# Kernel tuning notes

Hardware: AMD Instinct MI355X
Metric: run time of the kernel (lower is better)

Reference implementation:

```python
import jax, jax.numpy as jnp
import numpy as np

B, S, D, H = 2, 2048, 1024, 16
HD = D // H  # 64


def setup_inputs() -> dict:
    key = jax.random.key(0)
    ks = jax.random.split(key, 11)
    sc = 1.0 / np.sqrt(D)
    return {
        "query": jax.random.normal(ks[0], (B, S, D), jnp.float32),
        "key_in": jax.random.normal(ks[1], (B, S, D), jnp.float32),
        "value_in": jax.random.normal(ks[2], (B, S, D), jnp.float32),
        "mask": jnp.ones((1, 1, S, S), dtype=bool),
        "Wq": jax.random.normal(ks[3], (D, D), jnp.float32) * sc,
        "bq": jnp.zeros((D,), jnp.float32),
        "Wk": jax.random.normal(ks[4], (D, D), jnp.float32) * sc,
        "bk": jnp.zeros((D,), jnp.float32),
        "Wv": jax.random.normal(ks[5], (D, D), jnp.float32) * sc,
        "bv": jnp.zeros((D,), jnp.float32),
        "Wo": jax.random.normal(ks[6], (D, D), jnp.float32) * sc,
        "bo": jnp.zeros((D,), jnp.float32),
    }


def _split_heads(x):
    b, s, _ = x.shape
    return x.reshape(b, s, H, HD).transpose(0, 2, 1, 3)  # [B,H,S,HD]


def reference(query, key_in, value_in, mask, Wq, bq, Wk, bk, Wv, bv, Wo, bo):
    # linear projections (torch Linear: x @ W.T + b)
    q = _split_heads(query @ Wq.T + bq)
    k = _split_heads(key_in @ Wk.T + bk)
    v = _split_heads(value_in @ Wv.T + bv)
    scores = jnp.einsum("bhqd,bhkd->bhqk", q, k) / np.sqrt(HD).astype(np.float32)
    scores = jnp.where(mask == 0, jnp.float32(-1e20), scores)
    probs = jax.nn.softmax(scores, axis=-1)
    attn = jnp.einsum("bhqk,bhkd->bhqd", probs, v)  # [B,H,S,HD]
    combined = attn.transpose(0, 2, 1, 3).reshape(query.shape[0], query.shape[1], H * HD)
    return combined @ Wo.T + bo
```

## Files before the change

### kernel.cpp

```cpp
#include <hip/hip_runtime.h>

#define B_  2
#define S_  2048
#define D_  1024
#define H_  16
#define HD_ 64

typedef float          f32x4 __attribute__((ext_vector_type(4)));
typedef short          s16x8 __attribute__((ext_vector_type(8)));
typedef unsigned short u16x4 __attribute__((ext_vector_type(4)));
typedef unsigned int   u32x4 __attribute__((ext_vector_type(4)));

static __device__ __forceinline__ unsigned short f2bf(float f) {
  unsigned int u = __builtin_bit_cast(unsigned int, f);
  u += 0x7FFFu + ((u >> 16) & 1u);
  return (unsigned short)(u >> 16);
}

#define GLDS16(g, l)                                                        \
  __builtin_amdgcn_global_load_lds(                                         \
      (const __attribute__((address_space(1))) void*)(g),                   \
      (__attribute__((address_space(3))) void*)(l), 16, 0, 0)

struct ConvSet {
  const float* s[4];
  unsigned short* d[4];
  int n[4];
};

__global__ __launch_bounds__(256) void conv_kernel(ConvSet cs) {
  const int idx = blockIdx.y;
  const int i = (blockIdx.x * 256 + threadIdx.x) * 8;
  if (i >= cs.n[idx]) return;
  const float* s = cs.s[idx];
  unsigned short* d = cs.d[idx];
  f32x4 a = *(const f32x4*)(s + i);
  f32x4 b = *(const f32x4*)(s + i + 4);
  u16x4 pa, pb;
#pragma unroll
  for (int j = 0; j < 4; ++j) { pa[j] = f2bf(a[j]); pb[j] = f2bf(b[j]); }
  *(u16x4*)(d + i) = pa;
  *(u16x4*)(d + i + 4) = pb;
}

template <int XM, bool PERM>
__global__ __launch_bounds__(256) void gemm_bf16(
    const void* __restrict__ X0, const void* __restrict__ X1,
    const void* __restrict__ X2,
    const unsigned short* __restrict__ W0, const unsigned short* __restrict__ W1,
    const unsigned short* __restrict__ W2,
    const float* __restrict__ b0, const float* __restrict__ b1, const float* __restrict__ b2,
    void* __restrict__ o0, void* __restrict__ o1, void* __restrict__ o2)
{
  constexpr int K = D_, N = D_;
  const int z = blockIdx.z;
  const void* X           = z == 0 ? X0 : (z == 1 ? X1 : X2);
  const unsigned short* W = z == 0 ? W0 : (z == 1 ? W1 : W2);
  const float* bias       = z == 0 ? b0 : (z == 1 ? b1 : b2);
  void* outp              = z == 0 ? o0 : (z == 1 ? o1 : o2);

  __shared__ unsigned short As[128][32];
  __shared__ unsigned short Bs[128][32];

  const int t = threadIdx.x, lane = t & 63, w = t >> 6;
  const int wr = w >> 1, wc = w & 1;
  const int Lb = blockIdx.y * 8 + blockIdx.x;
  const int m0 = (Lb & 31) * 128;
  const int n0 = (Lb >> 5) * 128;
  const int lg = lane >> 4, lr = lane & 15;

  const int srow = w * 32 + (lane >> 2);
  const int scol = (lane & 3) * 8;
  const unsigned short* Bsrc = W + (size_t)(n0 + srow) * K + scol;
  const unsigned short* Asrc =
      (XM == 0) ? (const unsigned short*)X + (size_t)(m0 + srow) * K + scol : nullptr;

  f32x4 acc[4][4];
#pragma unroll
  for (int i = 0; i < 4; ++i)
#pragma unroll
    for (int j = 0; j < 4; ++j) acc[i][j] = f32x4{0.f, 0.f, 0.f, 0.f};

  for (int k0 = 0; k0 < K; k0 += 32) {
    __syncthreads();
    if (XM == 0) {
#pragma unroll
      for (int i = 0; i < 2; ++i)
        GLDS16(Asrc + k0 + (size_t)i * 16 * K, &As[w * 32 + i * 16][0]);
    } else {
      const float* Xf = (const float*)X;
#pragma unroll
      for (int i = 0; i < 4; ++i) {
        int c = t + 256 * i;
        int row = c >> 3, ko = (c & 7) * 4;
        f32x4 v = *(const f32x4*)(Xf + (size_t)(m0 + row) * K + k0 + ko);
        u16x4 p;
#pragma unroll
        for (int j = 0; j < 4; ++j) p[j] = f2bf(v[j]);
        *(u16x4*)&As[row][ko] = p;
      }
    }
#pragma unroll
    for (int i = 0; i < 2; ++i)
      GLDS16(Bsrc + k0 + (size_t)i * 16 * K, &Bs[w * 32 + i * 16][0]);
    __syncthreads();

    s16x8 af[4], bfr[4];
#pragma unroll
    for (int i = 0; i < 4; ++i) af[i]  = *(const s16x8*)&As[wr * 64 + i * 16 + lr][lg * 8];
#pragma unroll
    for (int j = 0; j < 4; ++j) bfr[j] = *(const s16x8*)&Bs[wc * 64 + j * 16 + lr][lg * 8];
#pragma unroll
    for (int i = 0; i < 4; ++i)
#pragma unroll
      for (int j = 0; j < 4; ++j)
        acc[i][j] = __builtin_amdgcn_mfma_f32_16x16x32_bf16(af[i], bfr[j], acc[i][j], 0, 0, 0);
  }

#pragma unroll
  for (int i = 0; i < 4; ++i) {
    int rowb = m0 + wr * 64 + i * 16 + lg * 4;
#pragma unroll
    for (int j = 0; j < 4; ++j) {
      int col = n0 + wc * 64 + j * 16 + lr;
      float bv = bias[col];
      if (PERM) {
        unsigned short* o = (unsigned short*)outp;
        int h = col >> 6, hd = col & (HD_ - 1);
        if (z == 2) {
          int b = rowb >> 11, sv = rowb & (S_ - 1);
          u16x4 pv;
#pragma unroll
          for (int r = 0; r < 4; ++r) pv[r] = f2bf(acc[i][j][r] + bv);
          *(u16x4*)(o + ((size_t)((b * H_ + h) * HD_ + hd)) * S_ + sv) = pv;
        } else {
#pragma unroll
          for (int r = 0; r < 4; ++r) {
            int rr = rowb + r;
            int b = rr >> 11, s = rr & (S_ - 1);
            o[(((size_t)(b * H_ + h)) * S_ + s) * HD_ + hd] = f2bf(acc[i][j][r] + bv);
          }
        }
      } else {
#pragma unroll
        for (int r = 0; r < 4; ++r)
          ((float*)outp)[(size_t)(rowb + r) * N + col] = acc[i][j][r] + bv;
      }
    }
  }
}

template <bool XF32, bool PERM>
__global__ __launch_bounds__(256) void gemm_kernel(
    const void* __restrict__ X0, const void* __restrict__ X1, const void* __restrict__ X2,
    const float* __restrict__ W0, const float* __restrict__ W1, const float* __restrict__ W2,
    const float* __restrict__ b0, const float* __restrict__ b1, const float* __restrict__ b2,
    void* __restrict__ o0, void* __restrict__ o1, void* __restrict__ o2)
{
  constexpr int K = D_, N = D_;
  const int z = blockIdx.z;
  const void*  Xv   = z == 0 ? X0 : (z == 1 ? X1 : X2);
  const float* W    = z == 0 ? W0 : (z == 1 ? W1 : W2);
  const float* bias = z == 0 ? b0 : (z == 1 ? b1 : b2);
  void*        outp = z == 0 ? o0 : (z == 1 ? o1 : o2);

  __shared__ unsigned short As[128][32];
  __shared__ unsigned short Bs[128][32];

  const int t = threadIdx.x, lane = t & 63, w = t >> 6;
  const int wr = w >> 1, wc = w & 1;
  const int Lb = blockIdx.y * 8 + blockIdx.x;
  const int m0 = (Lb & 31) * 128;
  const int n0 = (Lb >> 5) * 128;
  const int lg = lane >> 4, lr = lane & 15;

  f32x4 acc[4][4];
#pragma unroll
  for (int i = 0; i < 4; ++i)
#pragma unroll
    for (int j = 0; j < 4; ++j) acc[i][j] = f32x4{0.f, 0.f, 0.f, 0.f};

  for (int k0 = 0; k0 < K; k0 += 32) {
    __syncthreads();
#pragma unroll
    for (int i = 0; i < 4; ++i) {
      int c = t + 256 * i;
      int row = c >> 3, ko = (c & 7) * 4;
      if (XF32) {
        const float* Xf = (const float*)Xv;
        f32x4 v = *(const f32x4*)(Xf + (size_t)(m0 + row) * K + k0 + ko);
        u16x4 p;
#pragma unroll
        for (int j = 0; j < 4; ++j) p[j] = f2bf(v[j]);
        *(u16x4*)&As[row][ko] = p;
      } else {
        const unsigned short* Xu = (const unsigned short*)Xv;
        *(u16x4*)&As[row][ko] = *(const u16x4*)(Xu + (size_t)(m0 + row) * K + k0 + ko);
      }
    }
#pragma unroll
    for (int i = 0; i < 4; ++i) {
      int c = t + 256 * i;
      int row = c >> 3, ko = (c & 7) * 4;
      f32x4 v = *(const f32x4*)(W + (size_t)(n0 + row) * K + k0 + ko);
      u16x4 p;
#pragma unroll
      for (int j = 0; j < 4; ++j) p[j] = f2bf(v[j]);
      *(u16x4*)&Bs[row][ko] = p;
    }
    __syncthreads();

    s16x8 af[4], bfr[4];
#pragma unroll
    for (int i = 0; i < 4; ++i) af[i]  = *(const s16x8*)&As[wr * 64 + i * 16 + lr][lg * 8];
#pragma unroll
    for (int j = 0; j < 4; ++j) bfr[j] = *(const s16x8*)&Bs[wc * 64 + j * 16 + lr][lg * 8];
#pragma unroll
    for (int i = 0; i < 4; ++i)
#pragma unroll
      for (int j = 0; j < 4; ++j)
        acc[i][j] = __builtin_amdgcn_mfma_f32_16x16x32_bf16(af[i], bfr[j], acc[i][j], 0, 0, 0);
  }

#pragma unroll
  for (int i = 0; i < 4; ++i) {
    int rowb = m0 + wr * 64 + i * 16 + lg * 4;
#pragma unroll
    for (int j = 0; j < 4; ++j) {
      int col = n0 + wc * 64 + j * 16 + lr;
      float bv = bias[col];
      if (PERM) {
        unsigned short* o = (unsigned short*)outp;
        int h = col >> 6, hd = col & (HD_ - 1);
        if (z == 2) {
          int b = rowb >> 11, sv = rowb & (S_ - 1);
          u16x4 pv;
#pragma unroll
          for (int r = 0; r < 4; ++r) pv[r] = f2bf(acc[i][j][r] + bv);
          *(u16x4*)(o + ((size_t)((b * H_ + h) * HD_ + hd)) * S_ + sv) = pv;
        } else {
#pragma unroll
          for (int r = 0; r < 4; ++r) {
            int rr = rowb + r;
            int b = rr >> 11, s = rr & (S_ - 1);
            o[(((size_t)(b * H_ + h)) * S_ + s) * HD_ + hd] = f2bf(acc[i][j][r] + bv);
          }
        }
      } else {
#pragma unroll
        for (int r = 0; r < 4; ++r)
          ((float*)outp)[(size_t)(rowb + r) * N + col] = acc[i][j][r] + bv;
      }
    }
  }
}

__global__ __launch_bounds__(256) void attn_kernel(
    const unsigned short* __restrict__ Q,
    const unsigned short* __restrict__ Kg,
    const unsigned short* __restrict__ VT,
    unsigned short* __restrict__ O)
{
  __shared__ unsigned short Ks[2][64][64];
  __shared__ unsigned short Vt[2][64][64];
  __shared__ unsigned int   Pw32[4][16][32];

  const int t = threadIdx.x, lane = t & 63, w = t >> 6;
  const int lg = lane >> 4, lr = lane & 15;
  const int Lb = blockIdx.y * 32 + blockIdx.x;
  const int bh = Lb & 31;
  const int qblk = Lb >> 5;
  const int q0 = qblk * 64 + w * 16;
  const size_t baseK = (size_t)bh * S_ * HD_;
  const size_t baseV = (size_t)bh * HD_ * S_;

  s16x8 qa[2];
#pragma unroll
  for (int kc = 0; kc < 2; ++kc)
    qa[kc] = *(const s16x8*)(Q + baseK + (size_t)(q0 + lr) * HD_ + kc * 32 + lg * 8);

  const int sub = lane >> 3;
  const int cg  = (lane & 7) ^ sub;
  const unsigned short* Ksrc = Kg + baseK + (size_t)(w * 16 + sub) * HD_ + cg * 8;
  const unsigned short* Vsrc = VT + baseV + (size_t)(w * 16 + sub) * S_  + cg * 8;

  f32x4 po[4];
#pragma unroll
  for (int nb = 0; nb < 4; ++nb) po[nb] = f32x4{0.f, 0.f, 0.f, 0.f};
  float m_r = -1e30f, l_r = 0.f;
  const float C2 = 0.18033688f;
  const int   xs = (lr & 7) * 8;
  const int   xw = (lr & 7) * 4;

  constexpr int NT = S_ / 64;

  {
    GLDS16(Ksrc,                    &Ks[0][w * 16][0]);
    GLDS16(Ksrc + 8 * HD_,          &Ks[0][w * 16 + 8][0]);
    GLDS16(Vsrc,                    &Vt[0][w * 16][0]);
    GLDS16(Vsrc + (size_t)8 * S_,   &Vt[0][w * 16 + 8][0]);
  }
  __syncthreads();

  for (int kt = 0; kt < NT; ++kt) {
    const int cur = kt & 1;
    if (kt + 1 < NT) {
      const int nxt = cur ^ 1;
      const size_t ko = (size_t)(kt + 1) * 64 * HD_;
      const size_t vo = (size_t)(kt + 1) * 64;
      GLDS16(Ksrc + ko,                  &Ks[nxt][w * 16][0]);
      GLDS16(Ksrc + ko + 8 * HD_,        &Ks[nxt][w * 16 + 8][0]);
      GLDS16(Vsrc + vo,                  &Vt[nxt][w * 16][0]);
      GLDS16(Vsrc + vo + (size_t)8 * S_, &Vt[nxt][w * 16 + 8][0]);
    }

    f32x4 sf[4];
    __builtin_amdgcn_s_setprio(1);
#pragma unroll
    for (int nb = 0; nb < 4; ++nb) {
      f32x4 a = f32x4{0.f, 0.f, 0.f, 0.f};
      int row = nb * 16 + lr;
#pragma unroll
      for (int kc = 0; kc < 2; ++kc) {
        s16x8 kb = *(const s16x8*)&Ks[cur][row][(kc * 32 + lg * 8) ^ xs];
        a = __builtin_amdgcn_mfma_f32_16x16x32_bf16(kb, qa[kc], a, 0, 0, 0);
      }
      sf[nb] = a;
    }
    __builtin_amdgcn_s_setprio(0);

    float mx = sf[0][0];
#pragma unroll
    for (int nb = 0; nb < 4; ++nb)
#pragma unroll
      for (int r = 0; r < 4; ++r) mx = fmaxf(mx, sf[nb][r]);
    mx = fmaxf(mx, __shfl_xor(mx, 16));
    mx = fmaxf(mx, __shfl_xor(mx, 32));
    float ms = mx * C2;
    bool grow = (ms - m_r) > 8.f;
    if (__any(grow)) {
      float mn = fmaxf(m_r, ms);
      float alpha = __builtin_amdgcn_exp2f(m_r - mn);
      m_r = mn;
      l_r *= alpha;
#pragma unroll
      for (int nb = 0; nb < 4; ++nb)
#pragma unroll
        for (int r = 0; r < 4; ++r) po[nb][r] *= alpha;
    }

    float pr[4][4];
    float rs = 0.f;
#pragma unroll
    for (int nb = 0; nb < 4; ++nb)
#pragma unroll
      for (int r = 0; r < 4; ++r) {
        float p = __builtin_amdgcn_exp2f(fmaf(sf[nb][r], C2, -m_r));
        pr[nb][r] = p;
        rs += p;
      }
    rs += __shfl_xor(rs, 16);
    rs += __shfl_xor(rs, 32);
    l_r += rs;

#pragma unroll
    for (int nb = 0; nb < 4; ++nb)
#pragma unroll
      for (int half = 0; half < 2; ++half) {
        unsigned pk = (unsigned)f2bf(pr[nb][2 * half]) |
                      ((unsigned)f2bf(pr[nb][2 * half + 1]) << 16);
        Pw32[w][lr][(nb * 8 + lg * 2 + half) ^ xw] = pk;
      }
    asm volatile("s_waitcnt lgkmcnt(0)" ::: "memory");
    __builtin_amdgcn_sched_barrier(0);
    s16x8 pa[2];
#pragma unroll
    for (int kc = 0; kc < 2; ++kc)
      pa[kc] = *(const s16x8*)&Pw32[w][lr][(kc * 16 + lg * 4) ^ xw];

    __builtin_amdgcn_s_setprio(1);
#pragma unroll
    for (int nb = 0; nb < 4; ++nb) {
      int d = nb * 16 + lr;
#pragma unroll
      for (int kc = 0; kc < 2; ++kc) {
        s16x8 vb = *(const s16x8*)&Vt[cur][d][(kc * 32 + lg * 8) ^ xs];
        po[nb] = __builtin_amdgcn_mfma_f32_16x16x32_bf16(vb, pa[kc], po[nb], 0, 0, 0);
      }
    }
    __builtin_amdgcn_s_setprio(0);

    __syncthreads();
  }

  unsigned* Ot = (unsigned*)&Ks[0][0][0];
  {
    float inv = __builtin_amdgcn_rcpf(l_r);
    const int qlocal = w * 16 + lr;
#pragma unroll
    for (int nb = 0; nb < 4; ++nb)
#pragma unroll
      for (int half = 0; half < 2; ++half) {
        unsigned pk = (unsigned)f2bf(po[nb][2 * half] * inv) |
                      ((unsigned)f2bf(po[nb][2 * half + 1] * inv) << 16);
        Ot[qlocal * 32 + ((nb * 8 + lg * 2 + half) ^ xw)] = pk;
      }
  }
  __syncthreads();
  {
    const int qp = t >> 2, ch = t & 3;
    const int xq = (qp & 7) * 4;
    u32x4 r0 = *(const u32x4*)&Ot[qp * 32 + ((ch * 8) ^ xq)];
    u32x4 r1 = *(const u32x4*)&Ot[qp * 32 + ((ch * 8 + 4) ^ xq)];
    const int b = bh >> 4, h = bh & (H_ - 1);
    size_t s = (size_t)qblk * 64 + qp;
    unsigned short* o = O + ((size_t)b * S_ + s) * D_ + h * HD_ + ch * 16;
    *(u32x4*)o = r0;
    *(u32x4*)(o + 8) = r1;
  }
}

extern "C" void kernel_launch(void* const* d_in, const int* in_sizes, int n_in,
                              void* d_out, int out_size, void* d_ws, size_t ws_size,
                              hipStream_t stream) {
  const float* query    = (const float*)d_in[0];
  const float* key_in   = (const float*)d_in[1];
  const float* value_in = (const float*)d_in[2];
  const float* Wq = (const float*)d_in[4];
  const float* bq = (const float*)d_in[5];
  const float* Wk = (const float*)d_in[6];
  const float* bk = (const float*)d_in[7];
  const float* Wv = (const float*)d_in[8];
  const float* bv = (const float*)d_in[9];
  const float* Wo = (const float*)d_in[10];
  const float* bo = (const float*)d_in[11];

  const size_t NA = (size_t)B_ * S_ * D_;
  const size_t NW = (size_t)D_ * D_;
  dim3 blk(256);

  if (ws_size >= (4 * NA + 4 * NW) * sizeof(unsigned short)) {
    unsigned short* Wb[4];
    Wb[0] = (unsigned short*)d_ws;
    Wb[1] = Wb[0] + NW;
    Wb[2] = Wb[1] + NW;
    Wb[3] = Wb[2] + NW;
    unsigned short* Qp = Wb[3] + NW;
    unsigned short* Kp = Qp + NA;
    unsigned short* Vp = Kp + NA;
    unsigned short* Ao = Vp + NA;

    ConvSet cs;
    cs.s[0] = Wq; cs.d[0] = Wb[0]; cs.n[0] = (int)NW;
    cs.s[1] = Wk; cs.d[1] = Wb[1]; cs.n[1] = (int)NW;
    cs.s[2] = Wv; cs.d[2] = Wb[2]; cs.n[2] = (int)NW;
    cs.s[3] = Wo; cs.d[3] = Wb[3]; cs.n[3] = (int)NW;
    conv_kernel<<<dim3((unsigned)(NW / (256 * 8)), 4), blk, 0, stream>>>(cs);

    gemm_bf16<1, true><<<dim3(8, 32, 3), blk, 0, stream>>>(
        query, key_in, value_in, Wb[0], Wb[1], Wb[2], bq, bk, bv, Qp, Kp, Vp);
    attn_kernel<<<dim3(S_ / 64, B_ * H_), blk, 0, stream>>>(Qp, Kp, Vp, Ao);
    gemm_bf16<0, false><<<dim3(8, 32, 1), blk, 0, stream>>>(
        Ao, nullptr, nullptr, Wb[3], nullptr, nullptr, bo, nullptr, nullptr,
        (float*)d_out, nullptr, nullptr);
  } else {
    unsigned short* Qp = (unsigned short*)d_ws;
    unsigned short* Kp = Qp + NA;
    unsigned short* Vp = Kp + NA;
    unsigned short* Ao = Vp + NA;
    gemm_kernel<true, true><<<dim3(8, 32, 3), blk, 0, stream>>>(
        query, key_in, value_in, Wq, Wk, Wv, bq, bk, bv, Qp, Kp, Vp);
    attn_kernel<<<dim3(S_ / 64, B_ * H_), blk, 0, stream>>>(Qp, Kp, Vp, Ao);
    gemm_kernel<false, false><<<dim3(8, 32, 1), blk, 0, stream>>>(
        Ao, nullptr, nullptr, Wo, nullptr, nullptr, bo, nullptr, nullptr,
        (float*)d_out, nullptr, nullptr);
  }
}
```

Baseline: 296.2 us.

## Double-buffer LDS tiles in projection GEMM to overlap loads with MFMA

Splits the A and B shared-memory tiles into two buffers and prefetches the next K-slice while MFMAs run on the current one. For fp32 inputs, the global loads are issued before the compute and the bf16 conversion and LDS store happen after it. This cuts one barrier per iteration and hides global-load latency, at the cost of doubling LDS use and adding register pressure from the prefetched values.

```diff
diff --git a/kernel.cpp b/kernel.cpp
--- a/kernel.cpp
+++ b/kernel.cpp
@@ -53,14 +53,15 @@
     void* __restrict__ o0, void* __restrict__ o1, void* __restrict__ o2)
 {
   constexpr int K = D_, N = D_;
+  constexpr int NKS = K / 32;
   const int z = blockIdx.z;
   const void* X           = z == 0 ? X0 : (z == 1 ? X1 : X2);
   const unsigned short* W = z == 0 ? W0 : (z == 1 ? W1 : W2);
   const float* bias       = z == 0 ? b0 : (z == 1 ? b1 : b2);
   void* outp              = z == 0 ? o0 : (z == 1 ? o1 : o2);
 
-  __shared__ unsigned short As[128][32];
-  __shared__ unsigned short Bs[128][32];
+  __shared__ unsigned short As[2][128][32];
+  __shared__ unsigned short Bs[2][128][32];
 
   const int t = threadIdx.x, lane = t & 63, w = t >> 6;
   const int wr = w >> 1, wc = w & 1;
@@ -74,6 +75,9 @@
   const unsigned short* Bsrc = W + (size_t)(n0 + srow) * K + scol;
   const unsigned short* Asrc =
       (XM == 0) ? (const unsigned short*)X + (size_t)(m0 + srow) * K + scol : nullptr;
+  const int arow0 = t >> 3;
+  const int acol  = (t & 7) * 4;
+  const float* Xf = (XM == 1) ? (const float*)X : nullptr;
 
   f32x4 acc[4][4];
 #pragma unroll
@@ -81,40 +85,71 @@
 #pragma unroll
     for (int j = 0; j < 4; ++j) acc[i][j] = f32x4{0.f, 0.f, 0.f, 0.f};
 
-  for (int k0 = 0; k0 < K; k0 += 32) {
-    __syncthreads();
-    if (XM == 0) {
+  if (XM == 0) {
+#pragma unroll
+    for (int i = 0; i < 2; ++i)
+      GLDS16(Asrc + (size_t)i * 16 * K, &As[0][w * 32 + i * 16][0]);
+  } else {
+#pragma unroll
+    for (int i = 0; i < 4; ++i) {
+      f32x4 v = *(const f32x4*)(Xf + (size_t)(m0 + arow0 + 32 * i) * K + acol);
+      u16x4 p;
+#pragma unroll
+      for (int j = 0; j < 4; ++j) p[j] = f2bf(v[j]);
+      *(u16x4*)&As[0][arow0 + 32 * i][acol] = p;
+    }
+  }
+#pragma unroll
+  for (int i = 0; i < 2; ++i)
+    GLDS16(Bsrc + (size_t)i * 16 * K, &Bs[0][w * 32 + i * 16][0]);
+  __syncthreads();
+
+  for (int ks = 0; ks < NKS; ++ks) {
+    const int cur = ks & 1, nxt = cur ^ 1;
+    const int k1 = (ks + 1) * 32;
+
+    f32x4 av0, av1, av2, av3;
+    if (ks + 1 < NKS) {
+      if (XM == 0) {
+#pragma unroll
+        for (int i = 0; i < 2; ++i)
+          GLDS16(Asrc + k1 + (size_t)i * 16 * K, &As[nxt][w * 32 + i * 16][0]);
+      } else {
+        av0 = *(const f32x4*)(Xf + (size_t)(m0 + arow0)      * K + k1 + acol);
+        av1 = *(const f32x4*)(Xf + (size_t)(m0 + arow0 + 32) * K + k1 + acol);
+        av2 = *(const f32x4*)(Xf + (size_t)(m0 + arow0 + 64) * K + k1 + acol);
+        av3 = *(const f32x4*)(Xf + (size_t)(m0 + arow0 + 96) * K + k1 + acol);
+      }
 #pragma unroll
       for (int i = 0; i < 2; ++i)
-        GLDS16(Asrc + k0 + (size_t)i * 16 * K, &As[w * 32 + i * 16][0]);
-    } else {
-      const float* Xf = (const float*)X;
-#pragma unroll
-      for (int i = 0; i < 4; ++i) {
-        int c = t + 256 * i;
-        int row = c >> 3, ko = (c & 7) * 4;
-        f32x4 v = *(const f32x4*)(Xf + (size_t)(m0 + row) * K + k0 + ko);
-        u16x4 p;
-#pragma unroll
-        for (int j = 0; j < 4; ++j) p[j] = f2bf(v[j]);
-        *(u16x4*)&As[row][ko] = p;
-      }
-    }
-#pragma unroll
-    for (int i = 0; i < 2; ++i)
-      GLDS16(Bsrc + k0 + (size_t)i * 16 * K, &Bs[w * 32 + i * 16][0]);
-    __syncthreads();
+        GLDS16(Bsrc + k1 + (size_t)i * 16 * K, &Bs[nxt][w * 32 + i * 16][0]);
+    }
 
     s16x8 af[4], bfr[4];
 #pragma unroll
-    for (int i = 0; i < 4; ++i) af[i]  = *(const s16x8*)&As[wr * 64 + i * 16 + lr][lg * 8];
-#pragma unroll
-    for (int j = 0; j < 4; ++j) bfr[j] = *(const s16x8*)&Bs[wc * 64 + j * 16 + lr][lg * 8];
+    for (int i = 0; i < 4; ++i) af[i]  = *(const s16x8*)&As[cur][wr * 64 + i * 16 + lr][lg * 8];
+#pragma unroll
+    for (int j = 0; j < 4; ++j) bfr[j] = *(const s16x8*)&Bs[cur][wc * 64 + j * 16 + lr][lg * 8];
 #pragma unroll
     for (int i = 0; i < 4; ++i)
 #pragma unroll
       for (int j = 0; j < 4; ++j)
         acc[i][j] = __builtin_amdgcn_mfma_f32_16x16x32_bf16(af[i], bfr[j], acc[i][j], 0, 0, 0);
+
+    if (XM == 1 && ks + 1 < NKS) {
+      u16x4 p0, p1, p2, p3;
+#pragma unroll
+      for (int j = 0; j < 4; ++j) {
+        p0[j] = f2bf(av0[j]); p1[j] = f2bf(av1[j]);
+        p2[j] = f2bf(av2[j]); p3[j] = f2bf(av3[j]);
+      }
+      *(u16x4*)&As[nxt][arow0][acol]      = p0;
+      *(u16x4*)&As[nxt][arow0 + 32][acol] = p1;
+      *(u16x4*)&As[nxt][arow0 + 64][acol] = p2;
+      *(u16x4*)&As[nxt][arow0 + 96][acol] = p3;
+    }
+
+    __syncthreads();
   }
 
 #pragma unroll
```

Result: faster. 274.1 us (-7.5%).
